# Optimization experiments

Measured on AMD Instinct MI355X. Metric: run time of the kernel, lower is better.

## Reference

```python
import jax, jax.numpy as jnp
import numpy as np

N = 100000
E = 800000
IN_DIM = 128
HID = 128
OUT = 40
EPS = 1e-5


def setup_inputs() -> dict:
    key = jax.random.key(0)
    ks = jax.random.split(key, 12)
    inp = {
        "feat": jax.random.normal(ks[0], (N, IN_DIM), dtype=jnp.float32),
        "src": jax.random.randint(ks[1], (E,), 0, N, dtype=jnp.int32),
        "dst": jax.random.randint(ks[2], (E,), 0, N, dtype=jnp.int32),
        # layer 0: SAGEConv(IN_DIM -> HID), no bias; BN params
        "W_self0": jax.random.normal(ks[3], (IN_DIM, HID), dtype=jnp.float32) / np.sqrt(IN_DIM),
        "W_neigh0": jax.random.normal(ks[4], (IN_DIM, HID), dtype=jnp.float32) / np.sqrt(IN_DIM),
        "gamma0": jnp.ones((HID,), dtype=jnp.float32),
        "beta0": jnp.zeros((HID,), dtype=jnp.float32),
        # layer 1: SAGEConv(HID -> HID), no bias; BN params
        "W_self1": jax.random.normal(ks[5], (HID, HID), dtype=jnp.float32) / np.sqrt(HID),
        "W_neigh1": jax.random.normal(ks[6], (HID, HID), dtype=jnp.float32) / np.sqrt(HID),
        "gamma1": jnp.ones((HID,), dtype=jnp.float32),
        "beta1": jnp.zeros((HID,), dtype=jnp.float32),
        # layer 2: SAGEConv(HID -> OUT), with bias
        "W_self2": jax.random.normal(ks[7], (HID, OUT), dtype=jnp.float32) / np.sqrt(HID),
        "W_neigh2": jax.random.normal(ks[8], (HID, OUT), dtype=jnp.float32) / np.sqrt(HID),
        "b2": jnp.zeros((OUT,), dtype=jnp.float32),
    }
    return inp


def _sage_conv(h, src, dst, W_self, W_neigh, bias=None):
    # DGL SAGEConv with 'mean' aggregation: mean over in-neighbors, then
    # fc_self(h) + fc_neigh(h_neigh) (+ bias).
    msg = h[src]  # [E, d] gather of source-node features
    agg = jax.ops.segment_sum(msg, dst, num_segments=N)  # [N, d]
    deg = jax.ops.segment_sum(jnp.ones((src.shape[0],), h.dtype), dst, num_segments=N)
    h_neigh = agg / jnp.maximum(deg, 1.0)[:, None]
    out = h @ W_self + h_neigh @ W_neigh
    if bias is not None:
        out = out + bias
    return out


def _batch_norm(h, gamma, beta):
    # BatchNorm1d training-mode forward: batch statistics over nodes (axis 0).
    mean = jnp.mean(h, axis=0)
    var = jnp.mean(jnp.square(h - mean), axis=0)
    return (h - mean) * jax.lax.rsqrt(var + EPS) * gamma + beta


def reference(feat, src, dst,
              W_self0, W_neigh0, gamma0, beta0,
              W_self1, W_neigh1, gamma1, beta1,
              W_self2, W_neigh2, b2):
    # dropout layers are identity in eval mode
    h = feat
    h = _sage_conv(h, src, dst, W_self0, W_neigh0)
    h = jax.nn.relu(_batch_norm(h, gamma0, beta0))
    h = _sage_conv(h, src, dst, W_self1, W_neigh1)
    h = jax.nn.relu(_batch_norm(h, gamma1, beta1))
    h = _sage_conv(h, src, dst, W_self2, W_neigh2, bias=b2)
    return h
```

## Files before the change

### kernel.cpp

```cpp
#include <hip/hip_runtime.h>

#define N_NODES 100000
#define N_EDGES 800000
#define DIM 128
#define OUTD 40
#define OUTP 48
#define BN_EPS 1e-5f
#define SCAN_NB 98
#define NBKT 98
#define BKT_CAP 12288

typedef __bf16 bf16x8_t __attribute__((ext_vector_type(8)));
typedef float f32x4_t __attribute__((ext_vector_type(4)));
typedef float f32x2_t __attribute__((ext_vector_type(2)));

__device__ __forceinline__ unsigned short f2bf(float f) {
    unsigned int u = __builtin_bit_cast(unsigned int, f);
    u = (u + 0x7FFF + ((u >> 16) & 1)) >> 16;
    return (unsigned short)u;
}


__global__ __launch_bounds__(256) void bucketA_kernel(const int* __restrict__ src,
                                                      const int* __restrict__ dst,
                                                      uint2* __restrict__ pairs,
                                                      int* __restrict__ gcursor) {
    __shared__ int cnt[NBKT], base[NBKT], rec[NBKT];
    const int t = threadIdx.x;
    if (t < NBKT) { cnt[t] = 0; rec[t] = 0; }
    __syncthreads();
    const int e0 = blockIdx.x * 4096 + t * 16;
    const bool active = (e0 + 16 <= N_EDGES);
    int s[16], d[16];
    if (active) {
#pragma unroll
        for (int i = 0; i < 4; ++i) {
            int4 sv = *reinterpret_cast<const int4*>(&src[e0 + i * 4]);
            int4 dv = *reinterpret_cast<const int4*>(&dst[e0 + i * 4]);
            s[i * 4 + 0] = sv.x; s[i * 4 + 1] = sv.y; s[i * 4 + 2] = sv.z; s[i * 4 + 3] = sv.w;
            d[i * 4 + 0] = dv.x; d[i * 4 + 1] = dv.y; d[i * 4 + 2] = dv.z; d[i * 4 + 3] = dv.w;
        }
#pragma unroll
        for (int i = 0; i < 16; ++i) atomicAdd(&cnt[d[i] >> 10], 1);
    }
    __syncthreads();
    if (t < NBKT && cnt[t] > 0) base[t] = atomicAdd(&gcursor[t], cnt[t]);
    __syncthreads();
    if (active) {
#pragma unroll
        for (int i = 0; i < 16; ++i) {
            int bk = d[i] >> 10;
            int loc = atomicAdd(&rec[bk], 1);
            pairs[(size_t)bk * BKT_CAP + base[bk] + loc] = make_uint2((unsigned)s[i], (unsigned)d[i]);
        }
    }
}

__global__ __launch_bounds__(256) void phaseB_deg_kernel(const uint2* __restrict__ pairs,
                                                         const int* __restrict__ gcursor,
                                                         int* __restrict__ deg) {
    __shared__ int hist[1024];
    const int b = blockIdx.x;
    const int t = threadIdx.x;
#pragma unroll
    for (int j = 0; j < 4; ++j) hist[t * 4 + j] = 0;
    __syncthreads();
    const int m = gcursor[b];
    const uint2* __restrict__ bp = &pairs[(size_t)b * BKT_CAP];
    for (int i = t; i < m; i += 256) {
        uint2 p = bp[i];
        atomicAdd(&hist[p.y & 1023], 1);
    }
    __syncthreads();
    const int n0 = b << 10;
#pragma unroll
    for (int j = 0; j < 4; ++j) {
        int node = n0 + t * 4 + j;
        if (node < N_NODES) deg[node] = hist[t * 4 + j];
    }
}

__global__ __launch_bounds__(256) void scan_partial_kernel(const int* __restrict__ deg,
                                                           int* __restrict__ partials) {
    int b = blockIdx.x;
    int tid = threadIdx.x;
    int base = b * 1024 + tid * 4;
    int t0 = 0, t1 = 0, t2 = 0, t3 = 0;
    if (base + 3 < N_NODES) {
        int4 v = *reinterpret_cast<const int4*>(&deg[base]);
        t0 = v.x; t1 = v.y; t2 = v.z; t3 = v.w;
    } else {
        if (base + 0 < N_NODES) t0 = deg[base + 0];
        if (base + 1 < N_NODES) t1 = deg[base + 1];
        if (base + 2 < N_NODES) t2 = deg[base + 2];
        if (base + 3 < N_NODES) t3 = deg[base + 3];
    }
    int s = t0 + t1 + t2 + t3;
    __shared__ int red[256];
    red[tid] = s;
    __syncthreads();
    for (int o = 128; o; o >>= 1) {
        if (tid < o) red[tid] += red[tid + o];
        __syncthreads();
    }
    if (tid == 0) partials[b] = red[0];
}

__global__ __launch_bounds__(128) void scan_partials_kernel(int* __restrict__ partials) {
    __shared__ int s[128];
    int t = threadIdx.x;
    int v = (t < SCAN_NB) ? partials[t] : 0;
    s[t] = v;
    __syncthreads();
    for (int off = 1; off < 128; off <<= 1) {
        int u = (t >= off) ? s[t - off] : 0;
        __syncthreads();
        s[t] += u;
        __syncthreads();
    }
    if (t < SCAN_NB) partials[t] = s[t] - v;
}

__global__ __launch_bounds__(256) void scan_final_kernel(const int* __restrict__ deg,
                                                         const int* __restrict__ partials,
                                                         int* __restrict__ row_off) {
    int b = blockIdx.x;
    int tid = threadIdx.x;
    int base = b * 1024 + tid * 4;
    int t0 = 0, t1 = 0, t2 = 0, t3 = 0;
    if (base + 3 < N_NODES) {
        int4 v = *reinterpret_cast<const int4*>(&deg[base]);
        t0 = v.x; t1 = v.y; t2 = v.z; t3 = v.w;
    } else {
        if (base + 0 < N_NODES) t0 = deg[base + 0];
        if (base + 1 < N_NODES) t1 = deg[base + 1];
        if (base + 2 < N_NODES) t2 = deg[base + 2];
        if (base + 3 < N_NODES) t3 = deg[base + 3];
    }
    int s = t0 + t1 + t2 + t3;
    __shared__ int sc[256];
    sc[tid] = s;
    __syncthreads();
    for (int off = 1; off < 256; off <<= 1) {
        int u = (tid >= off) ? sc[tid - off] : 0;
        __syncthreads();
        sc[tid] += u;
        __syncthreads();
    }
    int run = partials[b] + sc[tid] - s;
    if (base + 0 < N_NODES) row_off[base + 0] = run; run += t0;
    if (base + 1 < N_NODES) row_off[base + 1] = run; run += t1;
    if (base + 2 < N_NODES) row_off[base + 2] = run; run += t2;
    if (base + 3 < N_NODES) row_off[base + 3] = run;
    if (b == 0 && tid == 0) row_off[N_NODES] = N_EDGES;
}

__global__ __launch_bounds__(256) void phaseC_fill_kernel(const uint2* __restrict__ pairs,
                                                          const int* __restrict__ gcursor,
                                                          const int* __restrict__ row_off,
                                                          int* __restrict__ csr_src) {
    __shared__ int cur[1024];
    const int b = blockIdx.x;
    const int t = threadIdx.x;
    const int n0 = b << 10;
#pragma unroll
    for (int j = 0; j < 4; ++j) {
        int node = n0 + t * 4 + j;
        if (node < N_NODES) cur[t * 4 + j] = row_off[node];
    }
    __syncthreads();
    const int m = gcursor[b];
    const uint2* __restrict__ bp = &pairs[(size_t)b * BKT_CAP];
    for (int i = t; i < m; i += 256) {
        uint2 p = bp[i];
        int pos = atomicAdd(&cur[p.y & 1023], 1);
        csr_src[pos] = (int)p.x;
    }
}


__global__ __launch_bounds__(256) void convert_bf16_kernel(const float* __restrict__ in,
                                                           unsigned short* __restrict__ out) {
    size_t i = (size_t)(blockIdx.x * blockDim.x + threadIdx.x) * 4;
    float4 v = *reinterpret_cast<const float4*>(&in[i]);
    ushort4 o;
    o.x = f2bf(v.x); o.y = f2bf(v.y); o.z = f2bf(v.z); o.w = f2bf(v.w);
    *reinterpret_cast<ushort4*>(&out[i]) = o;
}


__global__ __launch_bounds__(256) void wt_build_kernel(const float* __restrict__ Ws0,
                                                       const float* __restrict__ Wn0,
                                                       const float* __restrict__ Ws1,
                                                       const float* __restrict__ Wn1,
                                                       unsigned short* __restrict__ WT0,
                                                       unsigned short* __restrict__ WT1) {
    int e = blockIdx.x * blockDim.x + threadIdx.x;
    int layer = e >> 15;
    int r = e & 32767;
    int n = r >> 8;
    int k = r & 255;
    const float* Ws = layer ? Ws1 : Ws0;
    const float* Wn = layer ? Wn1 : Wn0;
    float v = (k < DIM) ? Ws[k * DIM + n] : Wn[(k - DIM) * DIM + n];
    unsigned short* WT = layer ? WT1 : WT0;
    WT[n * 256 + k] = f2bf(v);
}

__global__ __launch_bounds__(256) void wt2_build_kernel(const float* __restrict__ Ws2,
                                                        const float* __restrict__ Wn2,
                                                        unsigned short* __restrict__ WT2) {
    int e = blockIdx.x * blockDim.x + threadIdx.x;
    int n = e >> 8;
    int k = e & 255;
    float v = 0.f;
    if (n < OUTD) v = (k < DIM) ? Ws2[k * OUTD + n] : Wn2[(k - DIM) * OUTD + n];
    WT2[n * 256 + k] = f2bf(v);
}


__device__ __forceinline__ void unpack_add2(f32x2_t* a, uint4 v) {
    f32x2_t t0, t1, t2, t3;
    t0[0] = __builtin_bit_cast(float, v.x << 16);
    t0[1] = __builtin_bit_cast(float, v.x & 0xFFFF0000u);
    t1[0] = __builtin_bit_cast(float, v.y << 16);
    t1[1] = __builtin_bit_cast(float, v.y & 0xFFFF0000u);
    t2[0] = __builtin_bit_cast(float, v.z << 16);
    t2[1] = __builtin_bit_cast(float, v.z & 0xFFFF0000u);
    t3[0] = __builtin_bit_cast(float, v.w << 16);
    t3[1] = __builtin_bit_cast(float, v.w & 0xFFFF0000u);
    a[0] += t0;
    a[1] += t1;
    a[2] += t2;
    a[3] += t3;
}

__global__ __launch_bounds__(256) void agg_bf16_kernel(const unsigned short* __restrict__ h,
                                                       const int* __restrict__ row_off,
                                                       const int* __restrict__ csr_src,
                                                       unsigned short* __restrict__ hn) {
    int wave = threadIdx.x >> 6;
    int lane = threadIdx.x & 63;
    int node = blockIdx.x * 4 + wave;
    if (node >= N_NODES) return;
    int lo = row_off[node], hi = row_off[node + 1];
    const int grp = lane >> 4;
    const int l16 = lane & 15;
    f32x2_t a2[4];
#pragma unroll
    for (int q = 0; q < 4; ++q) a2[q] = (f32x2_t){0.f, 0.f};
    for (int base = lo; base < hi; base += 64) {
        int cnt = hi - base; if (cnt > 64) cnt = 64;
        int li = (lane < cnt) ? lane : (cnt - 1);
        int idx = csr_src[base + li];
        int nIter = (cnt + 7) >> 3;
        for (int k = 0; k < nIter; ++k) {
            int t0 = k * 8 + grp;
            int s0 = __shfl(idx, t0, 64);
            int s1 = __shfl(idx, t0 + 4, 64);
            if (t0 < cnt) {
                uint4 v0 = *reinterpret_cast<const uint4*>(&h[(size_t)s0 * DIM + l16 * 8]);
                unpack_add2(a2, v0);
            }
            if (t0 + 4 < cnt) {
                uint4 v1 = *reinterpret_cast<const uint4*>(&h[(size_t)s1 * DIM + l16 * 8]);
                unpack_add2(a2, v1);
            }
        }
    }
    float a[8] = {a2[0][0], a2[0][1], a2[1][0], a2[1][1],
                  a2[2][0], a2[2][1], a2[3][0], a2[3][1]};
#pragma unroll
    for (int q = 0; q < 8; ++q) {
        a[q] += __shfl_xor(a[q], 16, 64);
        a[q] += __shfl_xor(a[q], 32, 64);
    }
    if (grp == 0) {
        float rd = (hi > lo) ? 1.0f / (float)(hi - lo) : 1.0f;
        uint4 o;
        o.x = (unsigned int)f2bf(a[0] * rd) | ((unsigned int)f2bf(a[1] * rd) << 16);
        o.y = (unsigned int)f2bf(a[2] * rd) | ((unsigned int)f2bf(a[3] * rd) << 16);
        o.z = (unsigned int)f2bf(a[4] * rd) | ((unsigned int)f2bf(a[5] * rd) << 16);
        o.w = (unsigned int)f2bf(a[6] * rd) | ((unsigned int)f2bf(a[7] * rd) << 16);
        *reinterpret_cast<uint4*>(&hn[(size_t)node * DIM + l16 * 8]) = o;
    }
}


__global__ __launch_bounds__(256) void gemm_mfma_kernel(const unsigned short* __restrict__ Ab,
                                                        const unsigned short* __restrict__ Hb,
                                                        const unsigned short* __restrict__ WT,
                                                        unsigned short* __restrict__ C,
                                                        float* __restrict__ bnsum,
                                                        float* __restrict__ bnsq) {
    __shared__ unsigned short wt[16384];
    const int tid = threadIdx.x;
    const int wid = tid >> 6;
    const int lane = tid & 63;
    const int lrow = lane & 15;
    const int g = lane >> 4;
    const int r0 = blockIdx.x * 128 + wid * 32;

    bf16x8_t a[2][8];
#pragma unroll
    for (int ks = 0; ks < 8; ++ks) {
        const unsigned short* __restrict__ base = (ks < 4) ? Ab : Hb;
        const int kk = (ks & 3) * 32 + g * 8;
#pragma unroll
        for (int mt = 0; mt < 2; ++mt) {
            int row = r0 + mt * 16 + lrow;
            if (row >= N_NODES) row = N_NODES - 1;
            a[mt][ks] = *reinterpret_cast<const bf16x8_t*>(&base[(size_t)row * DIM + kk]);
        }
    }

    f32x4_t acc[2][8];
#pragma unroll
    for (int mt = 0; mt < 2; ++mt)
#pragma unroll
        for (int nt = 0; nt < 8; ++nt) acc[mt][nt] = (f32x4_t){0.f, 0.f, 0.f, 0.f};

#pragma unroll
    for (int hh = 0; hh < 2; ++hh) {
        if (hh) __syncthreads();
#pragma unroll
        for (int i = 0; i < 8; ++i) {
            int c = i * 256 + tid;
            int n = c >> 4;
            int koff = (c & 15) * 8;
            unsigned int waddr = ((unsigned int)(c * 16)) ^ (((unsigned int)(n & 7)) << 4);
            uint4 v = *reinterpret_cast<const uint4*>(&WT[n * 256 + hh * 128 + koff]);
            *reinterpret_cast<uint4*>(reinterpret_cast<char*>(wt) + waddr) = v;
        }
        __syncthreads();
#pragma unroll
        for (int ks = 0; ks < 4; ++ks) {
#pragma unroll
            for (int nt = 0; nt < 8; ++nt) {
                int n = nt * 16 + lrow;
                unsigned int raddr = ((unsigned int)(n * 256 + ks * 64 + g * 16)) ^ (((unsigned int)(n & 7)) << 4);
                bf16x8_t b = *reinterpret_cast<const bf16x8_t*>(reinterpret_cast<const char*>(wt) + raddr);
                acc[0][nt] = __builtin_amdgcn_mfma_f32_16x16x32_bf16(a[0][hh * 4 + ks], b, acc[0][nt], 0, 0, 0);
                acc[1][nt] = __builtin_amdgcn_mfma_f32_16x16x32_bf16(a[1][hh * 4 + ks], b, acc[1][nt], 0, 0, 0);
            }
        }
    }

    float ssum[8], ssq[8];
#pragma unroll
    for (int nt = 0; nt < 8; ++nt) { ssum[nt] = 0.f; ssq[nt] = 0.f; }
#pragma unroll
    for (int mt = 0; mt < 2; ++mt) {
#pragma unroll
        for (int j = 0; j < 4; ++j) {
            int row = r0 + mt * 16 + g * 4 + j;
            if (row < N_NODES) {
#pragma unroll
                for (int nt = 0; nt < 8; ++nt) {
                    float v = acc[mt][nt][j];
                    ssum[nt] += v;
                    ssq[nt] += v * v;
                }
            }
        }
    }
#pragma unroll
    for (int nt = 0; nt < 8; ++nt) {
        ssum[nt] += __shfl_xor(ssum[nt], 16, 64);
        ssum[nt] += __shfl_xor(ssum[nt], 32, 64);
        ssq[nt] += __shfl_xor(ssq[nt], 16, 64);
        ssq[nt] += __shfl_xor(ssq[nt], 32, 64);
    }
    __syncthreads();
    float* ls = reinterpret_cast<float*>(wt);
    float* lq = ls + 512;
    if (g == 0) {
#pragma unroll
        for (int nt = 0; nt < 8; ++nt) {
            ls[wid * 128 + nt * 16 + lrow] = ssum[nt];
            lq[wid * 128 + nt * 16 + lrow] = ssq[nt];
        }
    }
    __syncthreads();
    if (tid < 128) {
        float s = ls[tid] + ls[128 + tid] + ls[256 + tid] + ls[384 + tid];
        float q = lq[tid] + lq[128 + tid] + lq[256 + tid] + lq[384 + tid];
        atomicAdd(&bnsum[tid], s);
        atomicAdd(&bnsq[tid], q);
    }

#pragma unroll
    for (int mt = 0; mt < 2; ++mt) {
#pragma unroll
        for (int j = 0; j < 4; ++j) {
            int row = r0 + mt * 16 + g * 4 + j;
            if (row < N_NODES) {
#pragma unroll
                for (int nt = 0; nt < 8; ++nt)
                    C[(size_t)row * DIM + nt * 16 + lrow] = f2bf(acc[mt][nt][j]);
            }
        }
    }
}


__global__ __launch_bounds__(256) void bn_apply_bf16_kernel(unsigned short* __restrict__ H,
                                                            const float* __restrict__ bnsum,
                                                            const float* __restrict__ bnsq,
                                                            const float* __restrict__ gamma,
                                                            const float* __restrict__ beta) {
    size_t idx = (size_t)(blockIdx.x * blockDim.x + threadIdx.x) * 8;
    const float invN = 1.0f / (float)N_NODES;
    int c = (int)(idx & (DIM - 1));
    uint4 v = *reinterpret_cast<const uint4*>(&H[idx]);
    unsigned int w[4] = {v.x, v.y, v.z, v.w};
    uint4 o;
    unsigned int* op = &o.x;
#pragma unroll
    for (int p = 0; p < 4; ++p) {
        float x0 = __builtin_bit_cast(float, w[p] << 16);
        float x1 = __builtin_bit_cast(float, w[p] & 0xFFFF0000u);
        int c0 = c + p * 2, c1 = c0 + 1;
        float mean0 = bnsum[c0] * invN, mean1 = bnsum[c1] * invN;
        float var0 = bnsq[c0] * invN - mean0 * mean0;
        float var1 = bnsq[c1] * invN - mean1 * mean1;
        float y0 = (x0 - mean0) * gamma[c0] * rsqrtf(var0 + BN_EPS) + beta[c0];
        float y1 = (x1 - mean1) * gamma[c1] * rsqrtf(var1 + BN_EPS) + beta[c1];
        y0 = y0 > 0.f ? y0 : 0.f;
        y1 = y1 > 0.f ? y1 : 0.f;
        op[p] = (unsigned int)f2bf(y0) | ((unsigned int)f2bf(y1) << 16);
    }
    *reinterpret_cast<uint4*>(&H[idx]) = o;
}


__global__ __launch_bounds__(256) void gemm_out_mfma_kernel(const unsigned short* __restrict__ Ab,
                                                            const unsigned short* __restrict__ Hb,
                                                            const unsigned short* __restrict__ WT2,
                                                            const float* __restrict__ bias,
                                                            float* __restrict__ C) {
    __shared__ unsigned short wt[OUTP * 256];
    const int tid = threadIdx.x;

#pragma unroll
    for (int i = 0; i < 6; ++i) {
        int c = i * 256 + tid;
        int n = c >> 5;
        unsigned int waddr = ((unsigned int)(c * 16)) ^ (((unsigned int)(n & 7)) << 4);
        uint4 v = *reinterpret_cast<const uint4*>(&WT2[c * 8]);
        *reinterpret_cast<uint4*>(reinterpret_cast<char*>(wt) + waddr) = v;
    }
    __syncthreads();

    const int wid = tid >> 6;
    const int lane = tid & 63;
    const int lrow = lane & 15;
    const int g = lane >> 4;
    const int r0 = blockIdx.x * 128 + wid * 32;

    bf16x8_t a[2][8];
#pragma unroll
    for (int ks = 0; ks < 8; ++ks) {
        const unsigned short* __restrict__ base = (ks < 4) ? Ab : Hb;
        const int kk = (ks & 3) * 32 + g * 8;
#pragma unroll
        for (int mt = 0; mt < 2; ++mt) {
            int row = r0 + mt * 16 + lrow;
            if (row >= N_NODES) row = N_NODES - 1;
            a[mt][ks] = *reinterpret_cast<const bf16x8_t*>(&base[(size_t)row * DIM + kk]);
        }
    }

    f32x4_t acc[2][3];
#pragma unroll
    for (int mt = 0; mt < 2; ++mt)
#pragma unroll
        for (int nt = 0; nt < 3; ++nt) acc[mt][nt] = (f32x4_t){0.f, 0.f, 0.f, 0.f};

#pragma unroll
    for (int ks = 0; ks < 8; ++ks) {
#pragma unroll
        for (int nt = 0; nt < 3; ++nt) {
            int n = nt * 16 + lrow;
            unsigned int raddr = ((unsigned int)(n * 512 + ks * 64 + g * 16)) ^ (((unsigned int)(n & 7)) << 4);
            bf16x8_t b = *reinterpret_cast<const bf16x8_t*>(reinterpret_cast<const char*>(wt) + raddr);
            acc[0][nt] = __builtin_amdgcn_mfma_f32_16x16x32_bf16(a[0][ks], b, acc[0][nt], 0, 0, 0);
            acc[1][nt] = __builtin_amdgcn_mfma_f32_16x16x32_bf16(a[1][ks], b, acc[1][nt], 0, 0, 0);
        }
    }

    float bb[3];
#pragma unroll
    for (int nt = 0; nt < 3; ++nt) {
        int col = nt * 16 + lrow;
        bb[nt] = (col < OUTD) ? bias[col] : 0.f;
    }

#pragma unroll
    for (int mt = 0; mt < 2; ++mt) {
#pragma unroll
        for (int j = 0; j < 4; ++j) {
            int row = r0 + mt * 16 + g * 4 + j;
            if (row < N_NODES) {
#pragma unroll
                for (int nt = 0; nt < 3; ++nt) {
                    int col = nt * 16 + lrow;
                    if (col < OUTD)
                        C[(size_t)row * OUTD + col] = acc[mt][nt][j] + bb[nt];
                }
            }
        }
    }
}


extern "C" void kernel_launch(void* const* d_in, const int* in_sizes, int n_in,
                              void* d_out, int out_size, void* d_ws, size_t ws_size,
                              hipStream_t stream) {
    const float* feat = (const float*)d_in[0];
    const int* src = (const int*)d_in[1];
    const int* dst = (const int*)d_in[2];
    const float* Ws0 = (const float*)d_in[3];
    const float* Wn0 = (const float*)d_in[4];
    const float* g0  = (const float*)d_in[5];
    const float* be0 = (const float*)d_in[6];
    const float* Ws1 = (const float*)d_in[7];
    const float* Wn1 = (const float*)d_in[8];
    const float* g1  = (const float*)d_in[9];
    const float* be1 = (const float*)d_in[10];
    const float* Ws2 = (const float*)d_in[11];
    const float* Wn2 = (const float*)d_in[12];
    const float* b2  = (const float*)d_in[13];
    float* out = (float*)d_out;

    char* ws = (char*)d_ws;
    int*   gcursor = (int*)(ws);
    float* bn      = (float*)(ws + 512);
    int*   row_off = (int*)(ws + 2560);
    int*   partials= (int*)(ws + 402576);
    uint2* pairs   = (uint2*)(ws + 403200);
    int*   csr     = (int*)(ws + 10036992);
    int*   deg     = (int*)(ws + 13236992);
    unsigned short* featb = (unsigned short*)(ws + 13636992);
    unsigned short* hnb   = (unsigned short*)(ws + 39236992);
    unsigned short* h0b   = (unsigned short*)(ws + 64836992);
    unsigned short* WT0   = (unsigned short*)(ws + 90436992);
    unsigned short* WT1   = (unsigned short*)(ws + 90502528);
    unsigned short* WT2   = (unsigned short*)(ws + 90568064);
    unsigned short* h1b   = featb;

    hipMemsetAsync(ws, 0, 2560, stream);

    const int ABK = (N_EDGES + 4095) / 4096;
    const int AB = (N_NODES + 3) / 4;
    const int MB = (N_NODES + 127) / 128;
    const int NE = (N_NODES * DIM) / 4 / 256;
    const int NB8 = (N_NODES * DIM) / 8 / 256;

    bucketA_kernel<<<ABK, 256, 0, stream>>>(src, dst, pairs, gcursor);
    phaseB_deg_kernel<<<NBKT, 256, 0, stream>>>(pairs, gcursor, deg);
    scan_partial_kernel<<<SCAN_NB, 256, 0, stream>>>(deg, partials);
    scan_partials_kernel<<<1, 128, 0, stream>>>(partials);
    scan_final_kernel<<<SCAN_NB, 256, 0, stream>>>(deg, partials, row_off);
    phaseC_fill_kernel<<<NBKT, 256, 0, stream>>>(pairs, gcursor, row_off, csr);

    convert_bf16_kernel<<<NE, 256, 0, stream>>>(feat, featb);
    wt_build_kernel<<<256, 256, 0, stream>>>(Ws0, Wn0, Ws1, Wn1, WT0, WT1);
    wt2_build_kernel<<<48, 256, 0, stream>>>(Ws2, Wn2, WT2);

    agg_bf16_kernel<<<AB, 256, 0, stream>>>(featb, row_off, csr, hnb);
    gemm_mfma_kernel<<<MB, 256, 0, stream>>>(featb, hnb, WT0, h0b, bn + 0, bn + 128);
    bn_apply_bf16_kernel<<<NB8, 256, 0, stream>>>(h0b, bn + 0, bn + 128, g0, be0);

    agg_bf16_kernel<<<AB, 256, 0, stream>>>(h0b, row_off, csr, hnb);
    gemm_mfma_kernel<<<MB, 256, 0, stream>>>(h0b, hnb, WT1, h1b, bn + 256, bn + 384);
    bn_apply_bf16_kernel<<<NB8, 256, 0, stream>>>(h1b, bn + 256, bn + 384, g1, be1);

    agg_bf16_kernel<<<AB, 256, 0, stream>>>(h1b, row_off, csr, hnb);
    gemm_out_mfma_kernel<<<MB, 256, 0, stream>>>(h1b, hnb, WT2, b2, out);
}
```

Before: 279.9 us.

## Map one node per 16-lane group in aggregation with unrolled 4-way gathers

The aggregation kernel now gives each 16-lane quarter-wave its own node instead of splitting one node's edges across a whole wave. This removes the cross-group shuffle reduction and the index-broadcast shuffles. Each group loads four neighbour indices and issues four 16-byte row gathers per iteration to keep more loads in flight. Groups in a wave run until the largest degree among the four nodes, so uneven degrees leave some lanes idle. The grid assumes N_NODES is divisible by 16, and clamped indices add a little extra load traffic.

```diff
diff --git a/kernel.cpp b/kernel.cpp
--- a/kernel.cpp
+++ b/kernel.cpp
@@ -239,51 +239,51 @@
                                                        const int* __restrict__ row_off,
                                                        const int* __restrict__ csr_src,
                                                        unsigned short* __restrict__ hn) {
-    int wave = threadIdx.x >> 6;
-    int lane = threadIdx.x & 63;
-    int node = blockIdx.x * 4 + wave;
-    if (node >= N_NODES) return;
-    int lo = row_off[node], hi = row_off[node + 1];
+    const int wave = threadIdx.x >> 6;
+    const int lane = threadIdx.x & 63;
     const int grp = lane >> 4;
     const int l16 = lane & 15;
+    const int node = blockIdx.x * 16 + wave * 4 + grp;
+    const int lo = row_off[node];
+    const int hi = row_off[node + 1];
+    const int cnt = hi - lo;
+    int mc = cnt;
+    mc = max(mc, __shfl_xor(mc, 16, 64));
+    mc = max(mc, __shfl_xor(mc, 32, 64));
+
     f32x2_t a2[4];
 #pragma unroll
     for (int q = 0; q < 4; ++q) a2[q] = (f32x2_t){0.f, 0.f};
-    for (int base = lo; base < hi; base += 64) {
-        int cnt = hi - base; if (cnt > 64) cnt = 64;
-        int li = (lane < cnt) ? lane : (cnt - 1);
-        int idx = csr_src[base + li];
-        int nIter = (cnt + 7) >> 3;
-        for (int k = 0; k < nIter; ++k) {
-            int t0 = k * 8 + grp;
-            int s0 = __shfl(idx, t0, 64);
-            int s1 = __shfl(idx, t0 + 4, 64);
-            if (t0 < cnt) {
-                uint4 v0 = *reinterpret_cast<const uint4*>(&h[(size_t)s0 * DIM + l16 * 8]);
-                unpack_add2(a2, v0);
-            }
-            if (t0 + 4 < cnt) {
-                uint4 v1 = *reinterpret_cast<const uint4*>(&h[(size_t)s1 * DIM + l16 * 8]);
-                unpack_add2(a2, v1);
-            }
-        }
-    }
-    float a[8] = {a2[0][0], a2[0][1], a2[1][0], a2[1][1],
-                  a2[2][0], a2[2][1], a2[3][0], a2[3][1]};
-#pragma unroll
-    for (int q = 0; q < 8; ++q) {
-        a[q] += __shfl_xor(a[q], 16, 64);
-        a[q] += __shfl_xor(a[q], 32, 64);
-    }
-    if (grp == 0) {
-        float rd = (hi > lo) ? 1.0f / (float)(hi - lo) : 1.0f;
-        uint4 o;
-        o.x = (unsigned int)f2bf(a[0] * rd) | ((unsigned int)f2bf(a[1] * rd) << 16);
-        o.y = (unsigned int)f2bf(a[2] * rd) | ((unsigned int)f2bf(a[3] * rd) << 16);
-        o.z = (unsigned int)f2bf(a[4] * rd) | ((unsigned int)f2bf(a[5] * rd) << 16);
-        o.w = (unsigned int)f2bf(a[6] * rd) | ((unsigned int)f2bf(a[7] * rd) << 16);
-        *reinterpret_cast<uint4*>(&hn[(size_t)node * DIM + l16 * 8]) = o;
-    }
+    const unsigned rowoff = (unsigned)l16 * 8u;
+
+    for (int t = 0; t < mc; t += 4) {
+        const bool p0 = t + 0 < cnt, p1 = t + 1 < cnt;
+        const bool p2 = t + 2 < cnt, p3 = t + 3 < cnt;
+        int i0 = csr_src[lo + min(t + 0, cnt > 0 ? cnt - 1 : 0)];
+        int i1 = csr_src[lo + min(t + 1, cnt > 0 ? cnt - 1 : 0)];
+        int i2 = csr_src[lo + min(t + 2, cnt > 0 ? cnt - 1 : 0)];
+        int i3 = csr_src[lo + min(t + 3, cnt > 0 ? cnt - 1 : 0)];
+        i0 = min(max(i0, 0), N_NODES - 1);
+        i1 = min(max(i1, 0), N_NODES - 1);
+        i2 = min(max(i2, 0), N_NODES - 1);
+        i3 = min(max(i3, 0), N_NODES - 1);
+        uint4 v0 = *reinterpret_cast<const uint4*>(&h[(size_t)i0 * DIM + rowoff]);
+        uint4 v1 = *reinterpret_cast<const uint4*>(&h[(size_t)i1 * DIM + rowoff]);
+        uint4 v2 = *reinterpret_cast<const uint4*>(&h[(size_t)i2 * DIM + rowoff]);
+        uint4 v3 = *reinterpret_cast<const uint4*>(&h[(size_t)i3 * DIM + rowoff]);
+        if (p0) unpack_add2(a2, v0);
+        if (p1) unpack_add2(a2, v1);
+        if (p2) unpack_add2(a2, v2);
+        if (p3) unpack_add2(a2, v3);
+    }
+
+    const float rd = (cnt > 0) ? 1.0f / (float)cnt : 1.0f;
+    uint4 o;
+    o.x = (unsigned int)f2bf(a2[0][0] * rd) | ((unsigned int)f2bf(a2[0][1] * rd) << 16);
+    o.y = (unsigned int)f2bf(a2[1][0] * rd) | ((unsigned int)f2bf(a2[1][1] * rd) << 16);
+    o.z = (unsigned int)f2bf(a2[2][0] * rd) | ((unsigned int)f2bf(a2[2][1] * rd) << 16);
+    o.w = (unsigned int)f2bf(a2[3][0] * rd) | ((unsigned int)f2bf(a2[3][1] * rd) << 16);
+    *reinterpret_cast<uint4*>(&hn[(size_t)node * DIM + rowoff]) = o;
 }
 
 
@@ -552,7 +552,7 @@
     hipMemsetAsync(ws, 0, 2560, stream);
 
     const int ABK = (N_EDGES + 4095) / 4096;
-    const int AB = (N_NODES + 3) / 4;
+    const int AGB = N_NODES / 16;
     const int MB = (N_NODES + 127) / 128;
     const int NE = (N_NODES * DIM) / 4 / 256;
     const int NB8 = (N_NODES * DIM) / 8 / 256;
@@ -568,14 +568,14 @@
     wt_build_kernel<<<256, 256, 0, stream>>>(Ws0, Wn0, Ws1, Wn1, WT0, WT1);
     wt2_build_kernel<<<48, 256, 0, stream>>>(Ws2, Wn2, WT2);
 
-    agg_bf16_kernel<<<AB, 256, 0, stream>>>(featb, row_off, csr, hnb);
+    agg_bf16_kernel<<<AGB, 256, 0, stream>>>(featb, row_off, csr, hnb);
     gemm_mfma_kernel<<<MB, 256, 0, stream>>>(featb, hnb, WT0, h0b, bn + 0, bn + 128);
     bn_apply_bf16_kernel<<<NB8, 256, 0, stream>>>(h0b, bn + 0, bn + 128, g0, be0);
 
-    agg_bf16_kernel<<<AB, 256, 0, stream>>>(h0b, row_off, csr, hnb);
+    agg_bf16_kernel<<<AGB, 256, 0, stream>>>(h0b, row_off, csr, hnb);
     gemm_mfma_kernel<<<MB, 256, 0, stream>>>(h0b, hnb, WT1, h1b, bn + 256, bn + 384);
     bn_apply_bf16_kernel<<<NB8, 256, 0, stream>>>(h1b, bn + 256, bn + 384, g1, be1);
 
-    agg_bf16_kernel<<<AB, 256, 0, stream>>>(h1b, row_off, csr, hnb);
+    agg_bf16_kernel<<<AGB, 256, 0, stream>>>(h1b, row_off, csr, hnb);
     gemm_out_mfma_kernel<<<MB, 256, 0, stream>>>(h1b, hnb, WT2, b2, out);
 }
```

Result: faster. 264.1 us (-5.7%).
